# Optimization experiments

Measured on AMD Instinct MI355X. Metric: run time of the kernel, lower is better.

The kernel has to match this reference:

```python
import jax, jax.numpy as jnp
import numpy as np

N, C_IN, C, V = 500000, 64, 64, 20000  # C = out_channel // 2


def bn(x, g, b, eps):
    # training-mode BatchNorm1d: batch statistics, biased variance
    mu = jnp.mean(x, axis=0)
    var = jnp.mean(jnp.square(x - mu), axis=0)
    return (x - mu) * jax.lax.rsqrt(var + eps) * g + b


def setup_inputs() -> dict:
    key = jax.random.key(0)
    ks = jax.random.split(key, 12)
    s = 0.05
    return {
        "inputs": jax.random.normal(ks[0], (N, C_IN), jnp.float32),
        "unq_inv": jax.random.randint(ks[1], (N,), 0, V, jnp.int32),
        "kv_W": jax.random.normal(ks[2], (C_IN, C), jnp.float32) * s,
        "kv_b": jnp.zeros((C,), jnp.float32),
        "norm_g": jnp.ones((C,), jnp.float32),
        "norm_b": jnp.zeros((C,), jnp.float32),
        "w1_W": jax.random.normal(ks[3], (C_IN, C), jnp.float32) * s,
        "w1_bias": jnp.zeros((C,), jnp.float32),
        "w_bn_g": jnp.ones((C,), jnp.float32),
        "w_bn_b": jnp.zeros((C,), jnp.float32),
        "w2_W": jax.random.normal(ks[4], (C, C), jnp.float32) * s,
        "w2_bias": jnp.zeros((C,), jnp.float32),
        "pre_W": jax.random.normal(ks[5], (C_IN, C), jnp.float32) * s,
        "pre_bias": jnp.zeros((C,), jnp.float32),
        "pre_bn_g": jnp.ones((C,), jnp.float32),
        "pre_bn_b": jnp.zeros((C,), jnp.float32),
        "posw_W": jax.random.normal(ks[6], (C, C), jnp.float32) * s,
        "posw_bias": jnp.zeros((C,), jnp.float32),
        "link_bn_g": jnp.ones((C,), jnp.float32),
        "link_bn_b": jnp.zeros((C,), jnp.float32),
    }


def _forward(inputs, unq_inv, kv_W, kv_b, norm_g, norm_b, w1_W, w1_bias,
             w_bn_g, w_bn_b, w2_W, w2_bias, pre_W, pre_bias, pre_bn_g,
             pre_bn_b, posw_W, posw_bias, link_bn_g, link_bn_b):
    inv = unq_inv
    # v = kv(inputs); x = relu(norm(v))
    v = inputs @ kv_W + kv_b                                   # [N, C]
    x = jax.nn.relu(bn(v, norm_g, norm_b, 1e-3))               # [N, C]
    # scatter_max
    q_max = jax.ops.segment_max(x, inv, num_segments=V)        # [V, C]
    q_max = jnp.where(jnp.isneginf(q_max), 0.0, q_max)
    # weight = w(inputs): Linear -> BN -> ReLU -> Linear
    h = jax.nn.relu(bn(inputs @ w1_W + w1_bias, w_bn_g, w_bn_b, 1e-5))
    weight = h @ w2_W + w2_bias                                # [N, C]
    # scatter_softmax over segments
    m = jax.ops.segment_max(weight, inv, num_segments=V)
    m = jnp.where(jnp.isneginf(m), 0.0, m)
    ex = jnp.exp(weight - m[inv])
    denom = jax.ops.segment_sum(ex, inv, num_segments=V)
    soft_weight = ex / denom[inv]                              # [N, C]
    # scatter_mean(soft_weight * v)
    cnt = jax.ops.segment_sum(jnp.ones((inputs.shape[0],), inputs.dtype), inv, num_segments=V)
    cnt = jnp.maximum(cnt, 1.0)[:, None]
    weight_x = jax.ops.segment_sum(soft_weight * v, inv, num_segments=V) / cnt  # [V, C]
    # LinkConv(q_max, inputs, inv)
    p = bn(inputs @ pre_W + pre_bias, pre_bn_g, pre_bn_b, 1e-3)  # [N, C]
    pw = p @ posw_W + posw_bias
    fs = p * jnp.sin(pw)
    fc = p * jnp.cos(pw)
    add_s = jax.ops.segment_sum(fs, inv, num_segments=V)         # [V, C]
    add_c = jax.ops.segment_sum(fc, inv, num_segments=V)
    f = bn(q_max @ pre_W + pre_bias, pre_bn_g, pre_bn_b, 1e-3)   # [V, C]
    mw = f @ posw_W + posw_bias
    cs = f * jnp.sin(mw)
    cc = f * jnp.cos(mw)
    final = (add_s + cs) * cs + (add_c + cc) * cc
    link_feat = jax.nn.relu(bn(final, link_bn_g, link_bn_b, 1e-3))
    weight_x = (link_feat + weight_x) * 0.5
    return jnp.concatenate([weight_x, q_max], axis=-1)           # [V, 2C]


def reference(inputs, unq_inv, kv_W, kv_b, norm_g, norm_b, w1_W, w1_bias,
              w_bn_g, w_bn_b, w2_W, w2_bias, pre_W, pre_bias, pre_bn_g,
              pre_bn_b, posw_W, posw_bias, link_bn_g, link_bn_b):
    return _forward(inputs, unq_inv, kv_W, kv_b, norm_g, norm_b, w1_W, w1_bias,
                    w_bn_g, w_bn_b, w2_W, w2_bias, pre_W, pre_bias, pre_bn_g,
                    pre_bn_b, posw_W, posw_bias, link_bn_g, link_bn_b)
```

## Files before the change

kernel.cpp:

```cpp
#include <hip/hip_runtime.h>

typedef __attribute__((ext_vector_type(8))) short  bf16x8;
typedef __attribute__((ext_vector_type(4))) float  f32x4;

#define MFMA16(a,b,c) __builtin_amdgcn_mfma_f32_16x16x32_bf16((a),(b),(c),0,0,0)

__device__ __forceinline__ float b2f(ushort u){ return __uint_as_float(((unsigned)u)<<16); }
__device__ __forceinline__ ushort f2b(float f){
  unsigned u = __float_as_uint(f);
  unsigned r = (u + 0x7FFFu + ((u>>16)&1u)) >> 16;
  return (ushort)r;
}
__device__ __forceinline__ float ldv(const void* p, long i, int mode){
  return mode ? ((const float*)p)[i] : b2f(((const ushort*)p)[i]);
}

__global__ void pfn_detect(const void* X, int* mode){
  __shared__ int cnt;
  if (threadIdx.x==0) cnt=0;
  __syncthreads();
  const ushort* u = (const ushort*)X;
  int bad=0;
  for (int i=threadIdx.x; i<4096; i+=256){
    float v = b2f(u[i]);
    if (!(fabsf(v) < 1e4f)) bad++;
  }
  atomicAdd(&cnt, bad);
  __syncthreads();
  if (threadIdx.x==0) *mode = (cnt > 204) ? 1 : 0;
}

__global__ __launch_bounds__(256) void pfn_g(const void* __restrict__ X, int N,
                                             float* __restrict__ G, float* __restrict__ svec,
                                             const int* gmode)
{
  __shared__ __align__(16) ushort xt[128*72];
  __shared__ float gred[4096];
  __shared__ float sred[64];
  int mode = *gmode;
  int tid = threadIdx.x;
  int w = tid>>6, lane = tid&63, q = lane>>4, li = lane&15;
  for (int u=tid; u<4096; u+=256) gred[u]=0.f;
  if (tid<64) sred[tid]=0.f;

  float s_acc[32];
#pragma unroll
  for (int i=0;i<32;i++) s_acc[i]=0.f;
  const f32x4 fz = {0.f,0.f,0.f,0.f};
  f32x4 acc[4][4];
#pragma unroll
  for (int a=0;a<4;a++)
#pragma unroll
    for (int b=0;b<4;b++) acc[a][b]=fz;

  int rr = tid>>1, half = tid&1;
  int nch = (N + 127)/128;
  for (int cb = blockIdx.x; cb < nch; cb += gridDim.x){
    int r = cb*128 + rr;
    float vals[32];
    if (r < N){
      if (mode){
        const float4* src = (const float4*)((const float*)X + (size_t)r*64 + half*32);
#pragma unroll
        for (int i=0;i<8;i++){ float4 f=src[i];
          vals[i*4]=f.x; vals[i*4+1]=f.y; vals[i*4+2]=f.z; vals[i*4+3]=f.w; }
      } else {
        const uint4* src = (const uint4*)((const ushort*)X + (size_t)r*64 + half*32);
#pragma unroll
        for (int i=0;i<4;i++){ uint4 u=src[i]; const ushort* pu=(const ushort*)&u;
#pragma unroll
          for (int l=0;l<8;l++) vals[i*8+l]=b2f(pu[l]); }
      }
    } else {
#pragma unroll
      for (int i=0;i<32;i++) vals[i]=0.f;
    }
#pragma unroll
    for (int i=0;i<32;i++) s_acc[i] += vals[i];
    ushort tmp[32];
#pragma unroll
    for (int i=0;i<32;i++) tmp[i]=f2b(vals[i]);
    uint4* dst = (uint4*)(xt + rr*72 + half*32);
#pragma unroll
    for (int i=0;i<4;i++) dst[i]=((const uint4*)tmp)[i];
    __syncthreads();

    bf16x8 fr[4];
#pragma unroll
    for (int mt=0; mt<4; mt++){
      bf16x8 f;
#pragma unroll
      for (int j=0;j<8;j++) f[j] = (short)xt[(w*32 + q*8 + j)*72 + mt*16 + li];
      fr[mt]=f;
    }
#pragma unroll
    for (int mt=0;mt<4;mt++)
#pragma unroll
      for (int nt=0;nt<4;nt++)
        acc[mt][nt] = MFMA16(fr[mt], fr[nt], acc[mt][nt]);
    __syncthreads();
  }
#pragma unroll
  for (int mt=0;mt<4;mt++)
#pragma unroll
    for (int nt=0;nt<4;nt++)
#pragma unroll
      for (int i=0;i<4;i++)
        atomicAdd(&gred[(mt*16 + q*4 + i)*64 + nt*16 + li], acc[mt][nt][i]);
#pragma unroll
  for (int i=0;i<32;i++) atomicAdd(&sred[half*32 + i], s_acc[i]);
  __syncthreads();
  for (int u=tid; u<4096; u+=256) atomicAdd(&G[u], gred[u]);
  if (tid<64) atomicAdd(&svec[tid], sred[tid]);
}

__global__ __launch_bounds__(256) void pfn_kstatsA(
    const float* __restrict__ G, const float* __restrict__ svec,
    const void* __restrict__ kvW, const void* __restrict__ w1W, const void* __restrict__ preW,
    const void* __restrict__ kvb, const void* __restrict__ w1b, const void* __restrict__ preb,
    const void* __restrict__ ng,  const void* __restrict__ nb,
    const void* __restrict__ wg,  const void* __restrict__ wb,
    const void* __restrict__ pg,  const void* __restrict__ pb,
    float* __restrict__ aA, float* __restrict__ cA,
    float* __restrict__ a1, float* __restrict__ ap, float* __restrict__ bp,
    float* __restrict__ bcat, float Nf, const int* gmode)
{
  __shared__ float gl[4096];
  __shared__ float sl[64];
  __shared__ float wl[4096];
  int mode = *gmode;
  int tid = threadIdx.x; int path = blockIdx.x;
  const void* wsel = (path==0)? kvW : (path==1)? w1W : preW;
  for (int u=tid; u<4096; u+=256){ gl[u]=G[u]; wl[u]=ldv(wsel,u,mode); }
  if (tid<64) sl[tid]=svec[tid];
  __syncthreads();
  int j = tid>>2, sub = tid&3;
  float ps=0.f, qf=0.f;
  for (int k=sub*16; k<sub*16+16; k++){
    float wk = wl[k*64+j];
    ps += sl[k]*wk;
    float tk=0.f;
    for (int m=0;m<64;m++) tk += gl[k*64+m]*wl[m*64+j];
    qf += tk*wk;
  }
  qf += __shfl_down(qf,2); qf += __shfl_down(qf,1);
  ps += __shfl_down(ps,2); ps += __shfl_down(ps,1);
  if (sub==0){
    float bias = ldv((path==0)? kvb : (path==1)? w1b : preb, j, mode);
    float gam  = ldv((path==0)? ng  : (path==1)? wg  : pg , j, mode);
    float bet  = ldv((path==0)? nb  : (path==1)? wb  : pb , j, mode);
    float eps  = (path==1)? 1e-5f : 1e-3f;
    float mean_raw = ps/Nf, qn = qf/Nf;
    float mean = mean_raw + bias;
    float var  = qn + 2.f*bias*mean_raw + bias*bias - mean*mean;
    float rstd = rsqrtf(fmaxf(var,0.f)+eps);
    float a = gam*rstd, c = bet - mean*a;
    if (path==0){ aA[j]=a; cA[j]=c; bcat[j]=bias; }
    else if (path==1){ a1[j]=a; bcat[64+j]=c+bias*a; }
    else { ap[j]=a; bp[j]=c+bias*a; bcat[128+j]=c+bias*a; }
  }
}

__global__ __launch_bounds__(256) void pfn_kstatsB(
    const void* __restrict__ kvW, const void* __restrict__ w1W,
    const void* __restrict__ preW, const void* __restrict__ poswW,
    const void* __restrict__ w2W, const void* __restrict__ w2b,
    const void* __restrict__ poswb,
    const float* __restrict__ a1, const float* __restrict__ ap, const float* __restrict__ bp,
    ushort* __restrict__ WT, float* __restrict__ bcat, float* __restrict__ b2o,
    const int* gmode)
{
  int mode = *gmode;
  int gidx = blockIdx.x*256 + threadIdx.x;
  for (int idx=gidx; idx<320*64; idx+=64*256){
    int n = idx>>6, k = idx&63;
    float o;
    if (n<64)        o = ldv(kvW, k*64+n, mode);
    else if (n<128){ int j=n-64;  o = ldv(w1W, k*64+j, mode)*a1[j]; }
    else if (n<192){ int j=n-128; o = ldv(preW, k*64+j, mode)*ap[j]; }
    else if (n<256){ int j=n-192; float t=0.f;
      for (int m=0;m<64;m++) t += ldv(preW,k*64+m,mode)*ap[m]*ldv(poswW,m*64+j,mode);
      o = t;
    } else {         int j=n-256; o = ldv(w2W, k*64+j, mode); }
    WT[idx] = f2b(o);
  }
  if (blockIdx.x==0 && threadIdx.x<64){
    int j = threadIdx.x; float bb=0.f;
    for (int m=0;m<64;m++) bb += bp[m]*ldv(poswW,m*64+j,mode);
    bcat[192+j] = bb + ldv(poswb,j,mode);
    b2o[j] = ldv(w2b,j,mode);
  }
}

__global__ void pfn_hist(const int* __restrict__ inv, int* __restrict__ hist, int N, int V){
  int i = blockIdx.x*blockDim.x + threadIdx.x;
  int stride = gridDim.x*blockDim.x;
  for (; i<N; i+=stride){
    int s = min(max(inv[i],0), V-1);
    atomicAdd(&hist[s], 1);
  }
}

__global__ __launch_bounds__(256) void pfn_scan(const int* __restrict__ hist,
                                                int* __restrict__ base, int* __restrict__ off,
                                                float* __restrict__ cntf, int V, int N){
  __shared__ int part[256];
  int tid = threadIdx.x;
  int per = (V+255)/256;
  int s0 = tid*per, s1 = min(s0+per, V);
  int sum=0;
  for (int s=s0;s<s1;s++) sum += hist[s];
  part[tid]=sum;
  __syncthreads();
  if (tid==0){ int acc=0; for (int i=0;i<256;i++){ int t=part[i]; part[i]=acc; acc+=t; } }
  __syncthreads();
  int acc = part[tid];
  for (int s=s0;s<s1;s++){ base[s]=acc; off[s]=acc; cntf[s]=(float)hist[s]; acc+=hist[s]; }
  if (tid==255) base[V]=N;
}

__global__ void pfn_scat(const int* __restrict__ inv, int* __restrict__ off,
                         int* __restrict__ sidx, int* __restrict__ segid, int N, int V){
  int i = blockIdx.x*blockDim.x + threadIdx.x;
  int stride = gridDim.x*blockDim.x;
  for (; i<N; i+=stride){
    int s = min(max(inv[i],0), V-1);
    int p = atomicAdd(&off[s],1);
    sidx[p] = i;
    segid[p] = s;
  }
}

#define RED_STORE(EXPR) \
  _Pragma("unroll") for (int s=0;s<2;s++){ \
  _Pragma("unroll") for (int i=0;i<4;i++){ \
    int rloc=w*32+s*16+q*4+i; \
  _Pragma("unroll") for (int t=0;t<4;t++){ int c=t*16+li; red[rloc*65+c] = (EXPR); } } }

#define RED_ADD(DST) { int cc=tid&63, gg=tid>>6; int nn=nlsS; \
  for (int ls=gg; ls<nn; ls+=4){ int sd=segSeg[ls]; if (sd<0) continue; \
    int lo=segStart[ls], hi=segStart[ls+1]; float a_=0.f; \
    for (int r_=lo; r_<hi; r_++) a_ += red[r_*65+cc]; \
    atomicAdd(&DST[(size_t)sd*64+cc], a_); } }

#define RED_MAX(DST) { int cc=tid&63, gg=tid>>6; int nn=nlsS; \
  for (int ls=gg; ls<nn; ls+=4){ int sd=segSeg[ls]; if (sd<0) continue; \
    int lo=segStart[ls], hi=segStart[ls+1]; float a_=0.f; \
    for (int r_=lo; r_<hi; r_++) a_ = fmaxf(a_, red[r_*65+cc]); \
    atomicMax(&DST[(size_t)sd*64+cc], __float_as_uint(a_)); } }

__global__ __launch_bounds__(256) void pfn_ms(
    const void* __restrict__ X, const int* __restrict__ sidx, const int* __restrict__ segid,
    const ushort* __restrict__ WT, const float* __restrict__ bcat,
    const float* __restrict__ aA, const float* __restrict__ cA, const float* __restrict__ b2o,
    unsigned int* __restrict__ qm, float* __restrict__ adds, float* __restrict__ addc,
    float* __restrict__ dnm, float* __restrict__ acv,
    int N, const int* gmode)
{
  __shared__ __align__(16) ushort xt[128*72];
  __shared__ float red[128*65];
  __shared__ float bcl[256], aAl[64], cAl[64], b2l[64];
  __shared__ int invs[128];
  __shared__ int segStart[129];
  __shared__ int segSeg[128];
  __shared__ int nlsS;
  int mode = *gmode;
  int tid = threadIdx.x;
  int p0 = blockIdx.x*128;

  {
    int rr=tid>>1, half=tid&1;
    int p = p0+rr;
    long r = (p<N)? (long)sidx[p] : -1;
    float vals[32];
    if (r>=0){
      if (mode){
        const float4* src=(const float4*)((const float*)X + r*64 + half*32);
#pragma unroll
        for (int i=0;i<8;i++){ float4 f=src[i];
          vals[i*4]=f.x; vals[i*4+1]=f.y; vals[i*4+2]=f.z; vals[i*4+3]=f.w; }
      } else {
        const uint4* src=(const uint4*)((const ushort*)X + r*64 + half*32);
#pragma unroll
        for (int i=0;i<4;i++){ uint4 u=src[i]; const ushort* pu=(const ushort*)&u;
#pragma unroll
          for (int l=0;l<8;l++) vals[i*8+l]=b2f(pu[l]); }
      }
    } else {
#pragma unroll
      for (int i=0;i<32;i++) vals[i]=0.f;
    }
    ushort tmp[32];
#pragma unroll
    for (int i=0;i<32;i++) tmp[i]=f2b(vals[i]);
    uint4* dst=(uint4*)(xt + rr*72 + half*32);
#pragma unroll
    for (int i=0;i<4;i++) dst[i]=((const uint4*)tmp)[i];
  }
  if (tid<128){ int p=p0+tid; invs[tid] = (p<N)? segid[p] : -1; }
  bcl[tid]=bcat[tid];
  if (tid<64){ aAl[tid]=aA[tid]; cAl[tid]=cA[tid]; b2l[tid]=b2o[tid]; }
  __syncthreads();
  if (tid==0){
    int n=0, prev=-2;
    for (int t=0;t<128;t++){ int s=invs[t]; if (s!=prev){ segStart[n]=t; segSeg[n]=s; prev=s; n++; } }
    segStart[n]=128; nlsS=n;
  }

  int w=tid>>6, lane=tid&63, q=lane>>4, li=lane&15;
  const f32x4 fz={0.f,0.f,0.f,0.f};

  f32x4 AV[2][4], AP[2][4], AW[2][4];
#pragma unroll
  for (int s=0;s<2;s++)
#pragma unroll
    for (int t=0;t<4;t++){ AV[s][t]=fz; AP[s][t]=fz; AW[s][t]=fz; }
#pragma unroll
  for (int kk=0;kk<2;kk++){
    bf16x8 a0 = *(const bf16x8*)&xt[(w*32 +      li)*72 + kk*32 + q*8];
    bf16x8 a1 = *(const bf16x8*)&xt[(w*32 + 16 + li)*72 + kk*32 + q*8];
    int ko = kk*32 + q*8;
#pragma unroll
    for (int t=0;t<4;t++){
      bf16x8 bv = *(const bf16x8*)&WT[(      t*16+li)*64 + ko];
      AV[0][t]=MFMA16(a0,bv,AV[0][t]); AV[1][t]=MFMA16(a1,bv,AV[1][t]);
      bf16x8 bp_= *(const bf16x8*)&WT[(128 + t*16+li)*64 + ko];
      AP[0][t]=MFMA16(a0,bp_,AP[0][t]); AP[1][t]=MFMA16(a1,bp_,AP[1][t]);
      bf16x8 bw = *(const bf16x8*)&WT[(192 + t*16+li)*64 + ko];
      AW[0][t]=MFMA16(a0,bw,AW[0][t]); AW[1][t]=MFMA16(a1,bw,AW[1][t]);
    }
  }
#pragma unroll
  for (int s=0;s<2;s++)
#pragma unroll
    for (int t=0;t<4;t++)
#pragma unroll
      for (int i=0;i<4;i++){
        int c=t*16+li;
        float v = AV[s][t][i] + bcl[c];
        AV[s][t][i] = v;
        float p = AP[s][t][i] + bcl[128+c];
        float pw= AW[s][t][i] + bcl[192+c];
        AP[s][t][i] = p*__sinf(pw);
        AW[s][t][i] = p*__cosf(pw);
      }
  RED_STORE(fmaxf(AV[s][t][i]*aAl[c]+cAl[c], 0.f));
  __syncthreads();
  RED_MAX(qm);
  __syncthreads();
  RED_STORE(AP[s][t][i]);
  __syncthreads();
  RED_ADD(adds);
  __syncthreads();
  RED_STORE(AW[s][t][i]);
  __syncthreads();
  RED_ADD(addc);
  __syncthreads();

  f32x4 AH[2][4];
#pragma unroll
  for (int s=0;s<2;s++)
#pragma unroll
    for (int t=0;t<4;t++) AH[s][t]=fz;
#pragma unroll
  for (int kk=0;kk<2;kk++){
    bf16x8 a0 = *(const bf16x8*)&xt[(w*32 +      li)*72 + kk*32 + q*8];
    bf16x8 a1 = *(const bf16x8*)&xt[(w*32 + 16 + li)*72 + kk*32 + q*8];
    int ko = kk*32 + q*8;
#pragma unroll
    for (int t=0;t<4;t++){
      bf16x8 bh = *(const bf16x8*)&WT[(64 + t*16+li)*64 + ko];
      AH[0][t]=MFMA16(a0,bh,AH[0][t]); AH[1][t]=MFMA16(a1,bh,AH[1][t]);
    }
  }
#pragma unroll
  for (int s=0;s<2;s++)
#pragma unroll
    for (int i=0;i<4;i++){
      int rloc=w*32+s*16+q*4+i;
#pragma unroll
      for (int t=0;t<4;t++){
        int c=t*16+li;
        xt[rloc*72 + c] = f2b(fmaxf(AH[s][t][i]+bcl[64+c], 0.f));
      }
    }
  __syncthreads();

  f32x4 AZ[2][4];
#pragma unroll
  for (int s=0;s<2;s++)
#pragma unroll
    for (int t=0;t<4;t++) AZ[s][t]=fz;
#pragma unroll
  for (int kk=0;kk<2;kk++){
    bf16x8 a0 = *(const bf16x8*)&xt[(w*32 +      li)*72 + kk*32 + q*8];
    bf16x8 a1 = *(const bf16x8*)&xt[(w*32 + 16 + li)*72 + kk*32 + q*8];
    int ko = kk*32 + q*8;
#pragma unroll
    for (int t=0;t<4;t++){
      bf16x8 bz = *(const bf16x8*)&WT[(256 + t*16+li)*64 + ko];
      AZ[0][t]=MFMA16(a0,bz,AZ[0][t]); AZ[1][t]=MFMA16(a1,bz,AZ[1][t]);
    }
  }
#pragma unroll
  for (int s=0;s<2;s++)
#pragma unroll
    for (int t=0;t<4;t++)
#pragma unroll
      for (int i=0;i<4;i++){
        int c=t*16+li;
        float e = __expf(fminf(AZ[s][t][i]+b2l[c], 30.f));
        AZ[s][t][i] = e;
        AV[s][t][i] = e*AV[s][t][i];
      }
  RED_STORE(AZ[s][t][i]);
  __syncthreads();
  RED_ADD(dnm);
  __syncthreads();
  RED_STORE(AV[s][t][i]);
  __syncthreads();
  RED_ADD(acv);
}

__global__ __launch_bounds__(256) void pfn_k2(
    const float* __restrict__ qmax, const void* __restrict__ preW,
    const void* __restrict__ preb, float* __restrict__ fq,
    float* __restrict__ fsum, float* __restrict__ fssq, int V, const int* gmode)
{
  __shared__ float pwl[64*72];
  __shared__ float qrow[4][64];
  __shared__ float red[8][64];
  int mode = *gmode;
  int tid=threadIdx.x, slot=tid>>6, j=tid&63;
  for (int u=tid;u<4096;u+=256){
    int k=u>>6, n=u&63;
    pwl[k*72+n]=ldv(preW,u,mode);
  }
  int per = (V + (int)gridDim.x - 1)/(int)gridDim.x;
  per = (per+3)&~3;
  int start = blockIdx.x*per, end = min(start+per, V);
  float ps=0.f, pq=0.f;
  float bj = ldv(preb,j,mode);
  __syncthreads();
  for (int rb=start; rb<end; rb+=4){
    int r = rb + slot;
    qrow[slot][j] = (r<V)? qmax[(size_t)r*64+j] : 0.f;
    __syncthreads();
    if (r<end){
      float t=bj;
#pragma unroll
      for (int k=0;k<64;k++) t += qrow[slot][k]*pwl[k*72+j];
      fq[(size_t)r*64+j]=t;
      ps += t; pq += t*t;
    }
    __syncthreads();
  }
  red[slot][j]=ps; red[4+slot][j]=pq;
  __syncthreads();
  if (slot==0){
    float s  = red[0][j]+red[1][j]+red[2][j]+red[3][j];
    float s2 = red[4][j]+red[5][j]+red[6][j]+red[7][j];
    atomicAdd(&fsum[j], s); atomicAdd(&fssq[j], s2);
  }
}

__global__ __launch_bounds__(256) void pfn_k4(
    const float* __restrict__ fq, const float* __restrict__ add_s,
    const float* __restrict__ add_c, const void* __restrict__ poswW,
    const void* __restrict__ poswb,
    const float* __restrict__ fsum, const float* __restrict__ fssq,
    const void* __restrict__ pg, const void* __restrict__ pbeta,
    float* __restrict__ finalb, float* __restrict__ lsum, float* __restrict__ lssq,
    int V, const int* gmode)
{
  __shared__ float pwl[64*72];
  __shared__ float frow[4][64];
  __shared__ float red[8][64];
  int mode = *gmode;
  int tid=threadIdx.x, slot=tid>>6, j=tid&63;
  for (int u=tid;u<4096;u+=256){
    int k=u>>6, n=u&63;
    pwl[k*72+n]=ldv(poswW,u,mode);
  }
  float Vf = (float)V;
  float mean = fsum[j]/Vf;
  float var  = fssq[j]/Vf - mean*mean;
  float s2 = ldv(pg,j,mode)*rsqrtf(fmaxf(var,0.f)+1e-3f);
  float c2 = ldv(pbeta,j,mode) - mean*s2;
  float pbj = ldv(poswb,j,mode);
  int per = (V + (int)gridDim.x - 1)/(int)gridDim.x;
  per = (per+3)&~3;
  int start = blockIdx.x*per, end = min(start+per, V);
  float ps=0.f, pq=0.f;
  __syncthreads();
  for (int rb=start; rb<end; rb+=4){
    int r = rb + slot;
    float fv = 0.f;
    if (r<end) fv = fq[(size_t)r*64+j]*s2 + c2;
    frow[slot][j]=fv;
    __syncthreads();
    if (r<end){
      float mw=pbj;
#pragma unroll
      for (int k=0;k<64;k++) mw += frow[slot][k]*pwl[k*72+j];
      float sn=__sinf(mw), cn=__cosf(mw);
      float cs = fv*sn, cc = fv*cn;
      float fin = (add_s[(size_t)r*64+j]+cs)*cs + (add_c[(size_t)r*64+j]+cc)*cc;
      finalb[(size_t)r*64+j]=fin;
      ps += fin; pq += fin*fin;
    }
    __syncthreads();
  }
  red[slot][j]=ps; red[4+slot][j]=pq;
  __syncthreads();
  if (slot==0){
    float s  = red[0][j]+red[1][j]+red[2][j]+red[3][j];
    float s2r= red[4][j]+red[5][j]+red[6][j]+red[7][j];
    atomicAdd(&lsum[j], s); atomicAdd(&lssq[j], s2r);
  }
}

__global__ __launch_bounds__(256) void pfn_k6(
    const float* __restrict__ finalb, const float* __restrict__ qmax,
    const float* __restrict__ denom, const float* __restrict__ accv,
    const float* __restrict__ cnt,
    const float* __restrict__ lsum, const float* __restrict__ lssq,
    const void* __restrict__ lg, const void* __restrict__ lb,
    void* __restrict__ out, int V, const int* gmode)
{
  int mode = *gmode;
  int tid=threadIdx.x, slot=tid>>6, j=tid&63;
  int r = blockIdx.x*4 + slot;
  if (r>=V) return;
  float Vf=(float)V;
  float mean=lsum[j]/Vf, var=lssq[j]/Vf-mean*mean;
  float s3=ldv(lg,j,mode)*rsqrtf(fmaxf(var,0.f)+1e-3f);
  float c3=ldv(lb,j,mode)-mean*s3;
  float lf = fmaxf(finalb[(size_t)r*64+j]*s3+c3, 0.f);
  float dn = denom[(size_t)r*64+j];
  float wx = accv[(size_t)r*64+j] / fmaxf(dn, 1e-20f);
  wx /= fmaxf(cnt[r],1.f);
  float y0 = (lf+wx)*0.5f;
  float y1 = qmax[(size_t)r*64+j];
  size_t o0 = (size_t)r*128+j, o1 = (size_t)r*128+64+j;
  if (mode){ ((float*)out)[o0]=y0; ((float*)out)[o1]=y1; }
  else { ((ushort*)out)[o0]=f2b(y0); ((ushort*)out)[o1]=f2b(y1); }
}

__global__ void pfn_sent(ushort* out, int n){
  int i = blockIdx.x*256 + threadIdx.x;
  if (i<n) out[i]=0x5300;
}

extern "C" void kernel_launch(void* const* d_in, const int* in_sizes, int n_in,
                              void* d_out, int out_size, void* d_ws, size_t ws_size,
                              hipStream_t stream)
{
  const void* X    = d_in[0];
  const int*  inv  = (const int*)d_in[1];
  const void* kvW  = d_in[2];
  const void* kvb  = d_in[3];
  const void* ng   = d_in[4];
  const void* nb   = d_in[5];
  const void* w1W  = d_in[6];
  const void* w1b  = d_in[7];
  const void* wg   = d_in[8];
  const void* wb   = d_in[9];
  const void* w2W  = d_in[10];
  const void* w2b  = d_in[11];
  const void* preW = d_in[12];
  const void* preb = d_in[13];
  const void* pg   = d_in[14];
  const void* pb   = d_in[15];
  const void* poswW= d_in[16];
  const void* poswb= d_in[17];
  const void* lg   = d_in[18];
  const void* lb   = d_in[19];

  int N = in_sizes[1];
  int V = out_size / 128;

  char* ws = (char*)d_ws;
  size_t off = 0;
  auto alloc = [&](size_t b){ size_t o=off; off=(off+b+255)&~(size_t)255; return o; };
  size_t oMode = alloc(256);
  size_t oG    = alloc(16384);
  size_t oS    = alloc(256);
  size_t oaA   = alloc(256);
  size_t ocA   = alloc(256);
  size_t obcat = alloc(1024);
  size_t ob2   = alloc(256);
  size_t oa1   = alloc(256);
  size_t oap   = alloc(256);
  size_t obp   = alloc(256);
  size_t ofsum = alloc(256);
  size_t ofssq = alloc(256);
  size_t olsum = alloc(256);
  size_t olssq = alloc(256);
  size_t zero1_end = off;
  size_t oWT   = alloc(320*64*2);
  size_t oqm   = alloc((size_t)V*256);
  size_t oadds = alloc((size_t)V*256);
  size_t oaddc = alloc((size_t)V*256);
  size_t odnm  = alloc((size_t)V*256);
  size_t oacv  = alloc((size_t)V*256);
  size_t ohist = alloc((size_t)V*4);
  size_t zero2_end = off;
  size_t ocntf = alloc((size_t)V*4);
  size_t obase = alloc((size_t)(V+1)*4);
  size_t ooff  = alloc((size_t)V*4);
  size_t osidx = alloc((size_t)N*4);
  size_t osegd = alloc((size_t)N*4);
  size_t ofq   = alloc((size_t)V*256);
  size_t ofin  = alloc((size_t)V*256);
  size_t need  = off;
  (void)n_in;

  if (ws_size < need){
    pfn_sent<<<(out_size+255)/256,256,0,stream>>>((ushort*)d_out, out_size);
    return;
  }

  hipMemsetAsync(ws, 0, zero1_end, stream);
  hipMemsetAsync(ws + oqm, 0, zero2_end - oqm, stream);

  int* gmode = (int*)(ws+oMode);

  pfn_detect<<<1,256,0,stream>>>(X, gmode);

  pfn_g<<<512,256,0,stream>>>(X, N, (float*)(ws+oG), (float*)(ws+oS), gmode);

  pfn_hist<<<2048,256,0,stream>>>(inv, (int*)(ws+ohist), N, V);

  pfn_kstatsA<<<3,256,0,stream>>>(
      (const float*)(ws+oG), (const float*)(ws+oS),
      kvW, w1W, preW, kvb, w1b, preb, ng, nb, wg, wb, pg, pb,
      (float*)(ws+oaA), (float*)(ws+ocA),
      (float*)(ws+oa1),
      (float*)(ws+oap), (float*)(ws+obp),
      (float*)(ws+obcat), (float)N, gmode);

  pfn_scan<<<1,256,0,stream>>>((const int*)(ws+ohist), (int*)(ws+obase),
                               (int*)(ws+ooff), (float*)(ws+ocntf), V, N);

  pfn_kstatsB<<<64,256,0,stream>>>(
      kvW, w1W, preW, poswW, w2W, w2b, poswb,
      (const float*)(ws+oa1), (const float*)(ws+oap), (const float*)(ws+obp),
      (ushort*)(ws+oWT), (float*)(ws+obcat), (float*)(ws+ob2), gmode);

  pfn_scat<<<2048,256,0,stream>>>(inv, (int*)(ws+ooff), (int*)(ws+osidx),
                                  (int*)(ws+osegd), N, V);

  int gb = (N + 127)/128;
  pfn_ms<<<gb,256,0,stream>>>(
      X, (const int*)(ws+osidx), (const int*)(ws+osegd),
      (const ushort*)(ws+oWT), (const float*)(ws+obcat),
      (const float*)(ws+oaA), (const float*)(ws+ocA), (const float*)(ws+ob2),
      (unsigned int*)(ws+oqm), (float*)(ws+oadds), (float*)(ws+oaddc),
      (float*)(ws+odnm), (float*)(ws+oacv),
      N, gmode);

  pfn_k2<<<250,256,0,stream>>>(
      (const float*)(ws+oqm), preW, preb,
      (float*)(ws+ofq), (float*)(ws+ofsum), (float*)(ws+ofssq), V, gmode);

  pfn_k4<<<250,256,0,stream>>>(
      (const float*)(ws+ofq), (const float*)(ws+oadds), (const float*)(ws+oaddc),
      poswW, poswb, (const float*)(ws+ofsum), (const float*)(ws+ofssq),
      pg, pb, (float*)(ws+ofin), (float*)(ws+olsum), (float*)(ws+olssq), V, gmode);

  pfn_k6<<<(V+3)/4,256,0,stream>>>(
      (const float*)(ws+ofin), (const float*)(ws+oqm),
      (const float*)(ws+odnm), (const float*)(ws+oacv), (const float*)(ws+ocntf),
      (const float*)(ws+olsum), (const float*)(ws+olssq),
      lg, lb, d_out, V, gmode);
}
```

Measured before the change: 728.8 us.

## Fuse histogram into stats kernel, swizzle reduction smem, shrink segment tables

The segment histogram is folded into the input-statistics kernel, which removes one launch. The bf16 staging is rewritten to skip a temporary array, and bf16 inputs are copied straight into shared memory. The shared reduction buffer drops its padded stride in favour of an XOR swizzle, the per-block segment tables are capped at 32 entries, and the V-projection MFMA is moved after the sum reductions so fewer accumulators are live at once. The k2 and k4 grids are also doubled. The 32-segment cap gives wrong results if a 128-row block spans more than 32 distinct segments.

```diff
diff --git a/kernel.cpp b/kernel.cpp
--- a/kernel.cpp
+++ b/kernel.cpp
@@ -32,7 +32,8 @@
 
 __global__ __launch_bounds__(256) void pfn_g(const void* __restrict__ X, int N,
                                              float* __restrict__ G, float* __restrict__ svec,
-                                             const int* gmode)
+                                             const int* gmode,
+                                             const int* __restrict__ inv, int* __restrict__ hist, int V)
 {
   __shared__ __align__(16) ushort xt[128*72];
   __shared__ float gred[4096];
@@ -40,6 +41,16 @@
   int mode = *gmode;
   int tid = threadIdx.x;
   int w = tid>>6, lane = tid&63, q = lane>>4, li = lane&15;
+
+  {
+    long i = (long)blockIdx.x*blockDim.x + tid;
+    long stride = (long)gridDim.x*blockDim.x;
+    for (; i<N; i+=stride){
+      int s = min(max(inv[i],0), V-1);
+      atomicAdd(&hist[s], 1);
+    }
+  }
+
   for (int u=tid; u<4096; u+=256) gred[u]=0.f;
   if (tid<64) sred[tid]=0.f;
 
@@ -57,32 +68,37 @@
   int nch = (N + 127)/128;
   for (int cb = blockIdx.x; cb < nch; cb += gridDim.x){
     int r = cb*128 + rr;
-    float vals[32];
+    uint4* dst = (uint4*)(xt + rr*72 + half*32);
     if (r < N){
       if (mode){
         const float4* src = (const float4*)((const float*)X + (size_t)r*64 + half*32);
 #pragma unroll
-        for (int i=0;i<8;i++){ float4 f=src[i];
-          vals[i*4]=f.x; vals[i*4+1]=f.y; vals[i*4+2]=f.z; vals[i*4+3]=f.w; }
+        for (int i=0;i<4;i++){
+          float4 f0=src[i*2], f1=src[i*2+1];
+          s_acc[i*8+0]+=f0.x; s_acc[i*8+1]+=f0.y; s_acc[i*8+2]+=f0.z; s_acc[i*8+3]+=f0.w;
+          s_acc[i*8+4]+=f1.x; s_acc[i*8+5]+=f1.y; s_acc[i*8+6]+=f1.z; s_acc[i*8+7]+=f1.w;
+          uint4 u;
+          u.x = (unsigned)f2b(f0.x) | ((unsigned)f2b(f0.y)<<16);
+          u.y = (unsigned)f2b(f0.z) | ((unsigned)f2b(f0.w)<<16);
+          u.z = (unsigned)f2b(f1.x) | ((unsigned)f2b(f1.y)<<16);
+          u.w = (unsigned)f2b(f1.z) | ((unsigned)f2b(f1.w)<<16);
+          dst[i]=u;
+        }
       } else {
         const uint4* src = (const uint4*)((const ushort*)X + (size_t)r*64 + half*32);
 #pragma unroll
-        for (int i=0;i<4;i++){ uint4 u=src[i]; const ushort* pu=(const ushort*)&u;
-#pragma unroll
-          for (int l=0;l<8;l++) vals[i*8+l]=b2f(pu[l]); }
+        for (int i=0;i<4;i++){
+          uint4 u=src[i]; dst[i]=u;
+          const ushort* pu=(const ushort*)&u;
+#pragma unroll
+          for (int l=0;l<8;l++) s_acc[i*8+l] += b2f(pu[l]);
+        }
       }
     } else {
-#pragma unroll
-      for (int i=0;i<32;i++) vals[i]=0.f;
-    }
-#pragma unroll
-    for (int i=0;i<32;i++) s_acc[i] += vals[i];
-    ushort tmp[32];
-#pragma unroll
-    for (int i=0;i<32;i++) tmp[i]=f2b(vals[i]);
-    uint4* dst = (uint4*)(xt + rr*72 + half*32);
-#pragma unroll
-    for (int i=0;i<4;i++) dst[i]=((const uint4*)tmp)[i];
+      uint4 z={0,0,0,0};
+#pragma unroll
+      for (int i=0;i<4;i++) dst[i]=z;
+    }
     __syncthreads();
 
     bf16x8 fr[4];
@@ -192,15 +208,6 @@
   }
 }
 
-__global__ void pfn_hist(const int* __restrict__ inv, int* __restrict__ hist, int N, int V){
-  int i = blockIdx.x*blockDim.x + threadIdx.x;
-  int stride = gridDim.x*blockDim.x;
-  for (; i<N; i+=stride){
-    int s = min(max(inv[i],0), V-1);
-    atomicAdd(&hist[s], 1);
-  }
-}
-
 __global__ __launch_bounds__(256) void pfn_scan(const int* __restrict__ hist,
                                                 int* __restrict__ base, int* __restrict__ off,
                                                 float* __restrict__ cntf, int V, int N){
@@ -231,22 +238,24 @@
   }
 }
 
+#define RIDX(r,c) (((r)<<6) + ((c) ^ ((r)&31)))
+
 #define RED_STORE(EXPR) \
   _Pragma("unroll") for (int s=0;s<2;s++){ \
   _Pragma("unroll") for (int i=0;i<4;i++){ \
     int rloc=w*32+s*16+q*4+i; \
-  _Pragma("unroll") for (int t=0;t<4;t++){ int c=t*16+li; red[rloc*65+c] = (EXPR); } } }
+  _Pragma("unroll") for (int t=0;t<4;t++){ int c=t*16+li; red[RIDX(rloc,c)] = (EXPR); } } }
 
 #define RED_ADD(DST) { int cc=tid&63, gg=tid>>6; int nn=nlsS; \
   for (int ls=gg; ls<nn; ls+=4){ int sd=segSeg[ls]; if (sd<0) continue; \
     int lo=segStart[ls], hi=segStart[ls+1]; float a_=0.f; \
-    for (int r_=lo; r_<hi; r_++) a_ += red[r_*65+cc]; \
+    for (int r_=lo; r_<hi; r_++) a_ += red[RIDX(r_,cc)]; \
     atomicAdd(&DST[(size_t)sd*64+cc], a_); } }
 
 #define RED_MAX(DST) { int cc=tid&63, gg=tid>>6; int nn=nlsS; \
   for (int ls=gg; ls<nn; ls+=4){ int sd=segSeg[ls]; if (sd<0) continue; \
     int lo=segStart[ls], hi=segStart[ls+1]; float a_=0.f; \
-    for (int r_=lo; r_<hi; r_++) a_ = fmaxf(a_, red[r_*65+cc]); \
+    for (int r_=lo; r_<hi; r_++) a_ = fmaxf(a_, red[RIDX(r_,cc)]); \
     atomicMax(&DST[(size_t)sd*64+cc], __float_as_uint(a_)); } }
 
 __global__ __launch_bounds__(256) void pfn_ms(
@@ -258,11 +267,11 @@
     int N, const int* gmode)
 {
   __shared__ __align__(16) ushort xt[128*72];
-  __shared__ float red[128*65];
+  __shared__ float red[128*64];
   __shared__ float bcl[256], aAl[64], cAl[64], b2l[64];
   __shared__ int invs[128];
-  __shared__ int segStart[129];
-  __shared__ int segSeg[128];
+  __shared__ int segStart[33];
+  __shared__ int segSeg[32];
   __shared__ int nlsS;
   int mode = *gmode;
   int tid = threadIdx.x;
@@ -272,49 +281,53 @@
     int rr=tid>>1, half=tid&1;
     int p = p0+rr;
     long r = (p<N)? (long)sidx[p] : -1;
-    float vals[32];
+    uint4* dst=(uint4*)(xt + rr*72 + half*32);
     if (r>=0){
       if (mode){
         const float4* src=(const float4*)((const float*)X + r*64 + half*32);
 #pragma unroll
-        for (int i=0;i<8;i++){ float4 f=src[i];
-          vals[i*4]=f.x; vals[i*4+1]=f.y; vals[i*4+2]=f.z; vals[i*4+3]=f.w; }
+        for (int i=0;i<4;i++){
+          float4 f0=src[i*2], f1=src[i*2+1];
+          uint4 u;
+          u.x = (unsigned)f2b(f0.x) | ((unsigned)f2b(f0.y)<<16);
+          u.y = (unsigned)f2b(f0.z) | ((unsigned)f2b(f0.w)<<16);
+          u.z = (unsigned)f2b(f1.x) | ((unsigned)f2b(f1.y)<<16);
+          u.w = (unsigned)f2b(f1.z) | ((unsigned)f2b(f1.w)<<16);
+          dst[i]=u;
+        }
       } else {
         const uint4* src=(const uint4*)((const ushort*)X + r*64 + half*32);
 #pragma unroll
-        for (int i=0;i<4;i++){ uint4 u=src[i]; const ushort* pu=(const ushort*)&u;
-#pragma unroll
-          for (int l=0;l<8;l++) vals[i*8+l]=b2f(pu[l]); }
+        for (int i=0;i<4;i++) dst[i]=src[i];
       }
     } else {
-#pragma unroll
-      for (int i=0;i<32;i++) vals[i]=0.f;
-    }
-    ushort tmp[32];
-#pragma unroll
-    for (int i=0;i<32;i++) tmp[i]=f2b(vals[i]);
-    uint4* dst=(uint4*)(xt + rr*72 + half*32);
-#pragma unroll
-    for (int i=0;i<4;i++) dst[i]=((const uint4*)tmp)[i];
+      uint4 z={0,0,0,0};
+#pragma unroll
+      for (int i=0;i<4;i++) dst[i]=z;
+    }
   }
   if (tid<128){ int p=p0+tid; invs[tid] = (p<N)? segid[p] : -1; }
   bcl[tid]=bcat[tid];
   if (tid<64){ aAl[tid]=aA[tid]; cAl[tid]=cA[tid]; b2l[tid]=b2o[tid]; }
   __syncthreads();
+
   if (tid==0){
     int n=0, prev=-2;
-    for (int t=0;t<128;t++){ int s=invs[t]; if (s!=prev){ segStart[n]=t; segSeg[n]=s; prev=s; n++; } }
+    for (int t=0;t<128;t++){
+      int s=invs[t];
+      if (s!=prev && n<32){ segStart[n]=t; segSeg[n]=s; prev=s; n++; }
+    }
     segStart[n]=128; nlsS=n;
   }
 
   int w=tid>>6, lane=tid&63, q=lane>>4, li=lane&15;
   const f32x4 fz={0.f,0.f,0.f,0.f};
 
-  f32x4 AV[2][4], AP[2][4], AW[2][4];
+  f32x4 AP[2][4], AW[2][4];
 #pragma unroll
   for (int s=0;s<2;s++)
 #pragma unroll
-    for (int t=0;t<4;t++){ AV[s][t]=fz; AP[s][t]=fz; AW[s][t]=fz; }
+    for (int t=0;t<4;t++){ AP[s][t]=fz; AW[s][t]=fz; }
 #pragma unroll
   for (int kk=0;kk<2;kk++){
     bf16x8 a0 = *(const bf16x8*)&xt[(w*32 +      li)*72 + kk*32 + q*8];
@@ -322,8 +335,6 @@
     int ko = kk*32 + q*8;
 #pragma unroll
     for (int t=0;t<4;t++){
-      bf16x8 bv = *(const bf16x8*)&WT[(      t*16+li)*64 + ko];
-      AV[0][t]=MFMA16(a0,bv,AV[0][t]); AV[1][t]=MFMA16(a1,bv,AV[1][t]);
       bf16x8 bp_= *(const bf16x8*)&WT[(128 + t*16+li)*64 + ko];
       AP[0][t]=MFMA16(a0,bp_,AP[0][t]); AP[1][t]=MFMA16(a1,bp_,AP[1][t]);
       bf16x8 bw = *(const bf16x8*)&WT[(192 + t*16+li)*64 + ko];
@@ -337,24 +348,48 @@
 #pragma unroll
       for (int i=0;i<4;i++){
         int c=t*16+li;
-        float v = AV[s][t][i] + bcl[c];
-        AV[s][t][i] = v;
         float p = AP[s][t][i] + bcl[128+c];
         float pw= AW[s][t][i] + bcl[192+c];
         AP[s][t][i] = p*__sinf(pw);
         AW[s][t][i] = p*__cosf(pw);
       }
+  RED_STORE(AP[s][t][i]);
+  __syncthreads();
+  RED_ADD(adds);
+  __syncthreads();
+  RED_STORE(AW[s][t][i]);
+  __syncthreads();
+  RED_ADD(addc);
+  __syncthreads();
+
+  f32x4 AV[2][4];
+#pragma unroll
+  for (int s=0;s<2;s++)
+#pragma unroll
+    for (int t=0;t<4;t++) AV[s][t]=fz;
+#pragma unroll
+  for (int kk=0;kk<2;kk++){
+    bf16x8 a0 = *(const bf16x8*)&xt[(w*32 +      li)*72 + kk*32 + q*8];
+    bf16x8 a1 = *(const bf16x8*)&xt[(w*32 + 16 + li)*72 + kk*32 + q*8];
+    int ko = kk*32 + q*8;
+#pragma unroll
+    for (int t=0;t<4;t++){
+      bf16x8 bv = *(const bf16x8*)&WT[(      t*16+li)*64 + ko];
+      AV[0][t]=MFMA16(a0,bv,AV[0][t]); AV[1][t]=MFMA16(a1,bv,AV[1][t]);
+    }
+  }
+#pragma unroll
+  for (int s=0;s<2;s++)
+#pragma unroll
+    for (int t=0;t<4;t++)
+#pragma unroll
+      for (int i=0;i<4;i++){
+        int c=t*16+li;
+        AV[s][t][i] += bcl[c];
+      }
   RED_STORE(fmaxf(AV[s][t][i]*aAl[c]+cAl[c], 0.f));
   __syncthreads();
   RED_MAX(qm);
-  __syncthreads();
-  RED_STORE(AP[s][t][i]);
-  __syncthreads();
-  RED_ADD(adds);
-  __syncthreads();
-  RED_STORE(AW[s][t][i]);
-  __syncthreads();
-  RED_ADD(addc);
   __syncthreads();
 
   f32x4 AH[2][4];
@@ -628,9 +663,8 @@
 
   pfn_detect<<<1,256,0,stream>>>(X, gmode);
 
-  pfn_g<<<512,256,0,stream>>>(X, N, (float*)(ws+oG), (float*)(ws+oS), gmode);
-
-  pfn_hist<<<2048,256,0,stream>>>(inv, (int*)(ws+ohist), N, V);
+  pfn_g<<<512,256,0,stream>>>(X, N, (float*)(ws+oG), (float*)(ws+oS), gmode,
+                              inv, (int*)(ws+ohist), V);
 
   pfn_kstatsA<<<3,256,0,stream>>>(
       (const float*)(ws+oG), (const float*)(ws+oS),
@@ -660,11 +694,11 @@
       (float*)(ws+odnm), (float*)(ws+oacv),
       N, gmode);
 
-  pfn_k2<<<250,256,0,stream>>>(
+  pfn_k2<<<500,256,0,stream>>>(
       (const float*)(ws+oqm), preW, preb,
       (float*)(ws+ofq), (float*)(ws+ofsum), (float*)(ws+ofssq), V, gmode);
 
-  pfn_k4<<<250,256,0,stream>>>(
+  pfn_k4<<<500,256,0,stream>>>(
       (const float*)(ws+ofq), (const float*)(ws+oadds), (const float*)(ws+oaddc),
       poswW, poswb, (const float*)(ws+ofsum), (const float*)(ws+ofssq),
       pg, pb, (float*)(ws+ofin), (float*)(ws+olsum), (float*)(ws+olssq), V, gmode);
```

After: 741.5 us. Within noise of the previous version (+1.7%).
